# Performance work log

Hardware: AMD Instinct MI355X
Metric: run time of the kernel (lower is better)

Reference implementation:

```python
import jax, jax.numpy as jnp
import numpy as np

NUM_CLASSES = 1000
FEAT_DIM = 256
N = 262144
ALPHA = 0.5


def setup_inputs() -> dict:
    key = jax.random.key(0)
    k1, k2, k3 = jax.random.split(key, 3)
    features = jax.random.normal(k1, (N, FEAT_DIM), dtype=jnp.float32)
    labels = jax.random.randint(k2, (N,), 0, NUM_CLASSES, dtype=jnp.int64)
    centers = jax.random.normal(k3, (NUM_CLASSES, FEAT_DIM), dtype=jnp.float32)
    return {"features": features, "labels": labels, "centers": centers}


def reference(features, labels, centers):
    # Fused segment-mean: scatter-add of features + per-class counts,
    # replacing the per-class python loop in the original.
    sums = jax.ops.segment_sum(features, labels, num_segments=NUM_CLASSES)  # [C, D]
    counts = jax.ops.segment_sum(
        jnp.ones((features.shape[0],), dtype=features.dtype),
        labels,
        num_segments=NUM_CLASSES,
    )  # [C]
    has_samples = counts > 0
    safe_counts = jnp.where(has_samples, counts, 1.0)
    class_means = sums / safe_counts[:, None]  # [C, D]
    # EMA update only for classes present in the batch.
    updated = (1.0 - ALPHA) * centers + ALPHA * class_means
    new_centers = jnp.where(has_samples[:, None], updated, centers)
    return new_centers
```

## Files before the change

kernel.cpp:

```cpp
#include <hip/hip_runtime.h>

constexpr int N    = 262144;
constexpr int C    = 1000;
constexpr int D4   = 64;
constexpr int CPAD = 1024;
constexpr int NB   = 64;
constexpr int ROWS_PER_B = N / NB;
constexpr float ALPHA = 0.5f;

typedef float vfloat4 __attribute__((ext_vector_type(4)));


__global__ __launch_bounds__(256) void hist_kernel(
        const int* __restrict__ labels, int* __restrict__ hist) {
    __shared__ int h[CPAD];
    int t = threadIdx.x;
    for (int i = t; i < CPAD; i += 256) h[i] = 0;
    __syncthreads();
    int base = blockIdx.x * ROWS_PER_B;
    for (int i = t; i < ROWS_PER_B; i += 256)
        atomicAdd(&h[labels[base + i]], 1);
    __syncthreads();
    int* out = hist + blockIdx.x * CPAD;
    for (int i = t; i < CPAD; i += 256) out[i] = h[i];
}

__global__ __launch_bounds__(1024) void scan_kernel(
        const int* __restrict__ hist,
        int* __restrict__ counts,
        int* __restrict__ offs,
        int* __restrict__ blockcursor) {
    __shared__ int s[CPAD];
    int t = threadIdx.x;
    int total = 0;
    #pragma unroll 8
    for (int b = 0; b < NB; ++b) total += hist[b * CPAD + t];
    counts[t] = total;
    s[t] = total;
    __syncthreads();
    for (int off = 1; off < CPAD; off <<= 1) {
        int add = (t >= off) ? s[t - off] : 0;
        __syncthreads();
        s[t] += add;
        __syncthreads();
    }
    int run = s[t] - total;
    offs[t] = run;
    for (int b = 0; b < NB; ++b) {
        blockcursor[b * CPAD + t] = run;
        run += hist[b * CPAD + t];
    }
}

__global__ __launch_bounds__(256) void scatter_kernel(
        const int* __restrict__ labels,
        const int* __restrict__ blockcursor,
        int* __restrict__ rowidx) {
    __shared__ int cur[CPAD];
    int t = threadIdx.x;
    const int* bc = blockcursor + blockIdx.x * CPAD;
    for (int i = t; i < CPAD; i += 256) cur[i] = bc[i];
    __syncthreads();
    int base = blockIdx.x * ROWS_PER_B;
    for (int i = t; i < ROWS_PER_B; i += 256) {
        int row = base + i;
        int pos = atomicAdd(&cur[labels[row]], 1);
        rowidx[pos] = row;
    }
}

__global__ __launch_bounds__(256) void class_reduce_kernel(
        const vfloat4* __restrict__ feat4,
        const float4* __restrict__ cen4,
        const int* __restrict__ offs,
        const int* __restrict__ counts,
        const int* __restrict__ rowidx,
        float4* __restrict__ out4) {
    int c     = blockIdx.x;
    int start = offs[c];
    int cnt   = counts[c];
    int wave  = threadIdx.x >> 6;
    int lane  = threadIdx.x & 63;
    int end   = start + cnt;

    vfloat4 acc[8];
    #pragma unroll
    for (int u = 0; u < 8; ++u) acc[u] = (vfloat4)0.f;

    int j = start + wave;
    for (; j + 28 < end; j += 32) {
        int r[8];
        #pragma unroll
        for (int u = 0; u < 8; ++u) r[u] = rowidx[j + 4 * u];
        #pragma unroll
        for (int u = 0; u < 8; ++u) {
            vfloat4 v = __builtin_nontemporal_load(&feat4[(long)r[u] * D4 + lane]);
            acc[u] += v;
        }
    }
    for (; j < end; j += 4) {
        int r = rowidx[j];
        vfloat4 v = __builtin_nontemporal_load(&feat4[(long)r * D4 + lane]);
        acc[0] += v;
    }
    #pragma unroll
    for (int u = 1; u < 8; ++u) acc[0] += acc[u];

    __shared__ float red[4][64][4];
    red[wave][lane][0] = acc[0].x;
    red[wave][lane][1] = acc[0].y;
    red[wave][lane][2] = acc[0].z;
    red[wave][lane][3] = acc[0].w;
    __syncthreads();

    if (wave == 0) {
        float sx = red[0][lane][0] + red[1][lane][0] + red[2][lane][0] + red[3][lane][0];
        float sy = red[0][lane][1] + red[1][lane][1] + red[2][lane][1] + red[3][lane][1];
        float sz = red[0][lane][2] + red[1][lane][2] + red[2][lane][2] + red[3][lane][2];
        float sw = red[0][lane][3] + red[1][lane][3] + red[2][lane][3] + red[3][lane][3];

        float4 cen = cen4[c * D4 + lane];
        float4 o;
        if (cnt > 0) {
            float s = ALPHA / (float)cnt;
            o.x = (1.0f - ALPHA) * cen.x + sx * s;
            o.y = (1.0f - ALPHA) * cen.y + sy * s;
            o.z = (1.0f - ALPHA) * cen.z + sz * s;
            o.w = (1.0f - ALPHA) * cen.w + sw * s;
        } else {
            o = cen;
        }
        out4[c * D4 + lane] = o;
    }
}

extern "C" void kernel_launch(void* const* d_in, const int* in_sizes, int n_in,
                              void* d_out, int out_size, void* d_ws, size_t ws_size,
                              hipStream_t stream) {
    const vfloat4* feat4  = (const vfloat4*)d_in[0];
    const int*     labels = (const int*)d_in[1];
    const float4*  cen4   = (const float4*)d_in[2];
    float4*        out4   = (float4*)d_out;

    int* hist        = (int*)d_ws;
    int* counts      = hist + NB * CPAD;
    int* offs        = counts + CPAD;
    int* blockcursor = offs + CPAD;
    int* rowidx      = blockcursor + NB * CPAD;

    hist_kernel<<<NB, 256, 0, stream>>>(labels, hist);
    scan_kernel<<<1, CPAD, 0, stream>>>(hist, counts, offs, blockcursor);
    scatter_kernel<<<NB, 256, 0, stream>>>(labels, blockcursor, rowidx);
    class_reduce_kernel<<<C, 256, 0, stream>>>(feat4, cen4, offs, counts, rowidx, out4);
}
```

Before: 363.0 us.

## Replace sort-based class gather with LDS atomic partial sums per feature chunk

Drops the four-kernel histogram, scan, scatter and per-class gather pipeline. In its place, one kernel has each block stream a row slice over a 32-float feature chunk and accumulate per-class sums and counts with shared-memory atomics. Bank-conflict swizzling keyed on the class index spreads those atomics. A second kernel reduces the 32 slice partials per class and applies the EMA update. This removes the serial single-block scan and the indirect row gathers, at the cost of about 132KB of LDS per block (one block per CU), heavy LDS atomic traffic, and a 32MB partials buffer written and reread.

New measurement: 635.7 us. +75.1%, slower.

```diff
diff --git a/kernel.cpp b/kernel.cpp
--- a/kernel.cpp
+++ b/kernel.cpp
@@ -1,155 +1,119 @@
 #include <hip/hip_runtime.h>
 
-constexpr int N    = 262144;
-constexpr int C    = 1000;
-constexpr int D4   = 64;
-constexpr int CPAD = 1024;
-constexpr int NB   = 64;
-constexpr int ROWS_PER_B = N / NB;
+constexpr int N  = 262144;
+constexpr int C  = 1000;
+constexpr int D  = 256;
+constexpr int D4 = 64;
+constexpr int NCHUNK = 8;
+constexpr int NSLICE = 32;
+constexpr int NBLK   = NCHUNK * NSLICE;
+constexpr int CHUNK_D  = D / NCHUNK;
+constexpr int CHUNK_D4 = CHUNK_D / 4;
+constexpr int ROWS_PER_SLICE = N / NSLICE;
+constexpr int ROWS_PER_WAVE  = ROWS_PER_SLICE / 8;
 constexpr float ALPHA = 0.5f;
 
 typedef float vfloat4 __attribute__((ext_vector_type(4)));
 
 
-__global__ __launch_bounds__(256) void hist_kernel(
-        const int* __restrict__ labels, int* __restrict__ hist) {
-    __shared__ int h[CPAD];
-    int t = threadIdx.x;
-    for (int i = t; i < CPAD; i += 256) h[i] = 0;
+__global__ __launch_bounds__(512, 2) void accum_kernel(
+        const vfloat4* __restrict__ feat4,
+        const int*     __restrict__ labels,
+        float*         __restrict__ partials,
+        int*           __restrict__ counts_p) {
+    __shared__ float lsum[C * CHUNK_D];
+    __shared__ int   lcnt[C];
+
+    const int bid   = blockIdx.x;
+    const int chunk = bid >> 5;
+    const int slice = bid & 31;
+    const int tid   = threadIdx.x;
+
+    for (int i = tid; i < C * CHUNK_D; i += 512) lsum[i] = 0.f;
+    for (int i = tid; i < C; i += 512) lcnt[i] = 0;
     __syncthreads();
-    int base = blockIdx.x * ROWS_PER_B;
-    for (int i = t; i < ROWS_PER_B; i += 256)
-        atomicAdd(&h[labels[base + i]], 1);
+
+    const int wave = tid >> 6;
+    const int lane = tid & 63;
+    const int rgrp = lane >> 3;
+    const int d8   = lane & 7;
+    const int col  = chunk * CHUNK_D4 + d8;
+    const int base = slice * ROWS_PER_SLICE + wave * ROWS_PER_WAVE + rgrp;
+    const bool do_count = (chunk == 0) && (d8 == 0);
+
+    for (int it = 0; it < ROWS_PER_WAVE / 8; it += 8) {
+        int     rows[8];
+        int     lab[8];
+        vfloat4 v[8];
+        #pragma unroll
+        for (int u = 0; u < 8; ++u) rows[u] = base + (it + u) * 8;
+        #pragma unroll
+        for (int u = 0; u < 8; ++u)
+            v[u] = __builtin_nontemporal_load(&feat4[(size_t)rows[u] * D4 + col]);
+        #pragma unroll
+        for (int u = 0; u < 8; ++u) lab[u] = labels[rows[u]];
+        #pragma unroll
+        for (int u = 0; u < 8; ++u) {
+            float* p  = &lsum[lab[u] * CHUNK_D];
+            const int d0 = d8 * 4;
+            const int sw = lab[u] & 31;
+            atomicAdd(&p[(d0 + 0 + sw) & 31], v[u].x);
+            atomicAdd(&p[(d0 + 1 + sw) & 31], v[u].y);
+            atomicAdd(&p[(d0 + 2 + sw) & 31], v[u].z);
+            atomicAdd(&p[(d0 + 3 + sw) & 31], v[u].w);
+            if (do_count) atomicAdd(&lcnt[lab[u]], 1);
+        }
+    }
+
     __syncthreads();
-    int* out = hist + blockIdx.x * CPAD;
-    for (int i = t; i < CPAD; i += 256) out[i] = h[i];
+    float* outp = partials + (size_t)bid * (C * CHUNK_D);
+    for (int i = tid; i < C * CHUNK_D; i += 512) {
+        const int cls = i >> 5;
+        const int dd  = i & 31;
+        outp[i] = lsum[cls * CHUNK_D + ((dd + cls) & 31)];
+    }
+    if (chunk == 0)
+        for (int i = tid; i < C; i += 512)
+            counts_p[slice * C + i] = lcnt[i];
 }
 
-__global__ __launch_bounds__(1024) void scan_kernel(
-        const int* __restrict__ hist,
-        int* __restrict__ counts,
-        int* __restrict__ offs,
-        int* __restrict__ blockcursor) {
-    __shared__ int s[CPAD];
-    int t = threadIdx.x;
-    int total = 0;
-    #pragma unroll 8
-    for (int b = 0; b < NB; ++b) total += hist[b * CPAD + t];
-    counts[t] = total;
-    s[t] = total;
-    __syncthreads();
-    for (int off = 1; off < CPAD; off <<= 1) {
-        int add = (t >= off) ? s[t - off] : 0;
-        __syncthreads();
-        s[t] += add;
-        __syncthreads();
+__global__ __launch_bounds__(256) void finalize_kernel(
+        const float* __restrict__ partials,
+        const int*   __restrict__ counts_p,
+        const float* __restrict__ centers,
+        float*       __restrict__ out) {
+    const int c     = blockIdx.x;
+    const int d     = threadIdx.x;
+    const int chunk = d >> 5;
+    const int dd    = d & 31;
+
+    float s = 0.f;
+    #pragma unroll
+    for (int sl = 0; sl < NSLICE; ++sl) {
+        const int b = (chunk << 5) | sl;
+        s += partials[(size_t)b * (C * CHUNK_D) + c * CHUNK_D + dd];
     }
-    int run = s[t] - total;
-    offs[t] = run;
-    for (int b = 0; b < NB; ++b) {
-        blockcursor[b * CPAD + t] = run;
-        run += hist[b * CPAD + t];
-    }
-}
+    int cnt = 0;
+    #pragma unroll
+    for (int sl = 0; sl < NSLICE; ++sl) cnt += counts_p[sl * C + c];
 
-__global__ __launch_bounds__(256) void scatter_kernel(
-        const int* __restrict__ labels,
-        const int* __restrict__ blockcursor,
-        int* __restrict__ rowidx) {
-    __shared__ int cur[CPAD];
-    int t = threadIdx.x;
-    const int* bc = blockcursor + blockIdx.x * CPAD;
-    for (int i = t; i < CPAD; i += 256) cur[i] = bc[i];
-    __syncthreads();
-    int base = blockIdx.x * ROWS_PER_B;
-    for (int i = t; i < ROWS_PER_B; i += 256) {
-        int row = base + i;
-        int pos = atomicAdd(&cur[labels[row]], 1);
-        rowidx[pos] = row;
-    }
-}
-
-__global__ __launch_bounds__(256) void class_reduce_kernel(
-        const vfloat4* __restrict__ feat4,
-        const float4* __restrict__ cen4,
-        const int* __restrict__ offs,
-        const int* __restrict__ counts,
-        const int* __restrict__ rowidx,
-        float4* __restrict__ out4) {
-    int c     = blockIdx.x;
-    int start = offs[c];
-    int cnt   = counts[c];
-    int wave  = threadIdx.x >> 6;
-    int lane  = threadIdx.x & 63;
-    int end   = start + cnt;
-
-    vfloat4 acc[8];
-    #pragma unroll
-    for (int u = 0; u < 8; ++u) acc[u] = (vfloat4)0.f;
-
-    int j = start + wave;
-    for (; j + 28 < end; j += 32) {
-        int r[8];
-        #pragma unroll
-        for (int u = 0; u < 8; ++u) r[u] = rowidx[j + 4 * u];
-        #pragma unroll
-        for (int u = 0; u < 8; ++u) {
-            vfloat4 v = __builtin_nontemporal_load(&feat4[(long)r[u] * D4 + lane]);
-            acc[u] += v;
-        }
-    }
-    for (; j < end; j += 4) {
-        int r = rowidx[j];
-        vfloat4 v = __builtin_nontemporal_load(&feat4[(long)r * D4 + lane]);
-        acc[0] += v;
-    }
-    #pragma unroll
-    for (int u = 1; u < 8; ++u) acc[0] += acc[u];
-
-    __shared__ float red[4][64][4];
-    red[wave][lane][0] = acc[0].x;
-    red[wave][lane][1] = acc[0].y;
-    red[wave][lane][2] = acc[0].z;
-    red[wave][lane][3] = acc[0].w;
-    __syncthreads();
-
-    if (wave == 0) {
-        float sx = red[0][lane][0] + red[1][lane][0] + red[2][lane][0] + red[3][lane][0];
-        float sy = red[0][lane][1] + red[1][lane][1] + red[2][lane][1] + red[3][lane][1];
-        float sz = red[0][lane][2] + red[1][lane][2] + red[2][lane][2] + red[3][lane][2];
-        float sw = red[0][lane][3] + red[1][lane][3] + red[2][lane][3] + red[3][lane][3];
-
-        float4 cen = cen4[c * D4 + lane];
-        float4 o;
-        if (cnt > 0) {
-            float s = ALPHA / (float)cnt;
-            o.x = (1.0f - ALPHA) * cen.x + sx * s;
-            o.y = (1.0f - ALPHA) * cen.y + sy * s;
-            o.z = (1.0f - ALPHA) * cen.z + sz * s;
-            o.w = (1.0f - ALPHA) * cen.w + sw * s;
-        } else {
-            o = cen;
-        }
-        out4[c * D4 + lane] = o;
-    }
+    const float cen = centers[c * D + d];
+    float o = cen;
+    if (cnt > 0) o = (1.0f - ALPHA) * cen + s * (ALPHA / (float)cnt);
+    out[c * D + d] = o;
 }
 
 extern "C" void kernel_launch(void* const* d_in, const int* in_sizes, int n_in,
                               void* d_out, int out_size, void* d_ws, size_t ws_size,
                               hipStream_t stream) {
-    const vfloat4* feat4  = (const vfloat4*)d_in[0];
-    const int*     labels = (const int*)d_in[1];
-    const float4*  cen4   = (const float4*)d_in[2];
-    float4*        out4   = (float4*)d_out;
+    const vfloat4* feat4   = (const vfloat4*)d_in[0];
+    const int*     labels  = (const int*)d_in[1];
+    const float*   centers = (const float*)d_in[2];
+    float*         out     = (float*)d_out;
 
-    int* hist        = (int*)d_ws;
-    int* counts      = hist + NB * CPAD;
-    int* offs        = counts + CPAD;
-    int* blockcursor = offs + CPAD;
-    int* rowidx      = blockcursor + NB * CPAD;
+    float* partials = (float*)d_ws;
+    int*   counts_p = (int*)(partials + (size_t)NBLK * C * CHUNK_D);
 
-    hist_kernel<<<NB, 256, 0, stream>>>(labels, hist);
-    scan_kernel<<<1, CPAD, 0, stream>>>(hist, counts, offs, blockcursor);
-    scatter_kernel<<<NB, 256, 0, stream>>>(labels, blockcursor, rowidx);
-    class_reduce_kernel<<<C, 256, 0, stream>>>(feat4, cen4, offs, counts, rowidx, out4);
+    accum_kernel<<<NBLK, 512, 0, stream>>>(feat4, labels, partials, counts_p);
+    finalize_kernel<<<C, 256, 0, stream>>>(partials, counts_p, centers, out);
 }
```
